# Performance work log

Measured on AMD Instinct MI355X. Metric: run time of the kernel, lower is better.

Reference implementation:

```python
import jax, jax.numpy as jnp
import numpy as np

ROPE_THETA = 10000.0


def rope(t, rot_dim):
    """lucidrains-style rotary embedding: rotate first rot_dim features,
    interleaved (x0,x1) pairing; remaining features pass through.
    t: [B, S, D] with rot_dim <= D."""
    S = t.shape[-2]
    half = rot_dim // 2
    inv_freq = 1.0 / (ROPE_THETA ** (jnp.arange(0, rot_dim, 2, dtype=jnp.float32) / rot_dim))  # [half]
    freqs = jnp.arange(S, dtype=jnp.float32)[:, None] * inv_freq[None, :]  # [S, half]
    freqs = jnp.repeat(freqs, 2, axis=-1)  # [S, rot_dim]
    cos, sin = jnp.cos(freqs), jnp.sin(freqs)
    t_rot, t_pass = t[..., :rot_dim], t[..., rot_dim:]
    x = t_rot.reshape(*t_rot.shape[:-1], half, 2)
    rh = jnp.stack([-x[..., 1], x[..., 0]], axis=-1).reshape(t_rot.shape)  # rotate_half (interleaved)
    t_rot = t_rot * cos + rh * sin
    return jnp.concatenate([t_rot, t_pass], axis=-1)


def feature_map(x):
    # L2 normalize along the feature dim (Hydra-attention canonical choice)
    norm = jnp.sqrt(jnp.sum(x * x, axis=-1, keepdims=True))
    return x / jnp.maximum(norm, 1e-12)


def setup_inputs() -> dict:
    key = jax.random.key(0)
    kx, kwi, kwo = jax.random.split(key, 3)
    B, S, D = 8, 4096, 2048
    scale = 0.02  # keep activations numerically tame
    return {
        "X": jax.random.normal(kx, (B, S, D), dtype=jnp.float32),
        "W_in": jax.random.normal(kwi, (3 * D, D), dtype=jnp.float32) * scale,
        "b_in": jnp.zeros((3 * D,), dtype=jnp.float32),
        "W_out": jax.random.normal(kwo, (D, D), dtype=jnp.float32) * scale,
        "b_out": jnp.zeros((D,), dtype=jnp.float32),
    }


def reference(X, W_in, b_in, W_out, b_out):
    D = X.shape[-1]
    QKV = jnp.einsum("bsd,ed->bse", X, W_in) + b_in  # [B, S, 3D]
    Q, K, V = jnp.split(QKV, 3, axis=-1)
    rot_dim = D // 2  # RotaryEmbedding(feature_dim // 2)
    Q = rope(Q, rot_dim)
    K = rope(K, rot_dim)
    A = jnp.sum(feature_map(K) * V, axis=-2)  # [B, D] global sum over sequence
    Y = A[:, None, :] * Q  # [B, S, D]
    Y = jnp.einsum("bsd,ed->bse", Y, W_out) + b_out
    return Y + X
```

## Files before the change

kernel.cpp:

```cpp
#include <hip/hip_runtime.h>

#define N_TOK   32768L
#define DMODEL  2048L
#define E1      6144L
#define ROT     1024
#define SMASK   4095

typedef __attribute__((ext_vector_type(8))) _Float16 half8;
typedef __attribute__((ext_vector_type(4))) _Float16 half4;
typedef __attribute__((ext_vector_type(4))) float    floatx4;
typedef __attribute__((ext_vector_type(4))) float    float4v;

__device__ inline void gld16(const void* g, void* l) {
  __builtin_amdgcn_global_load_lds(
      (const __attribute__((address_space(1))) unsigned int*)g,
      (__attribute__((address_space(3))) unsigned int*)l,
      16, 0, 0);
}

__global__ __launch_bounds__(256) void k_f2h(const float* __restrict__ in,
                                             _Float16* __restrict__ out,
                                             long nElem) {
  long i = ((long)blockIdx.x * 256 + threadIdx.x) * 4;
  if (i + 3 < nElem) {
    float4v v = *(const float4v*)(in + i);
    half4 o;
    o[0] = (_Float16)v[0]; o[1] = (_Float16)v[1];
    o[2] = (_Float16)v[2]; o[3] = (_Float16)v[3];
    *(half4*)(out + i) = o;
  }
}

__global__ __launch_bounds__(256) void k_zero(float* __restrict__ p, int n) {
  int i = blockIdx.x * 256 + threadIdx.x;
  if (i < n) p[i] = 0.f;
}

__global__ __launch_bounds__(256) void k_tab(float2* __restrict__ tab) {
  int i = blockIdx.x * 256 + threadIdx.x;
  int s = i >> 9, j = i & 511;
  float invf = (float)pow(10000.0, -(double)j / 512.0);
  float ang  = (float)s * invf;
  double sd, cd; sincos((double)ang, &sd, &cd);
  float2 o; o.x = (float)cd; o.y = (float)sd;
  tab[i] = o;
}


#define MM(qm, qn) do { \
  _Pragma("unroll") for (int m4 = 0; m4 < 4; m4++) \
  _Pragma("unroll") for (int n2 = 0; n2 < 2; n2++) { \
    acc[(qm)*4+m4][(qn)*2+n2] = __builtin_amdgcn_mfma_f32_16x16x32_f16( \
        af[m4][0], bf[n2][0], acc[(qm)*4+m4][(qn)*2+n2], 0, 0, 0); \
    acc[(qm)*4+m4][(qn)*2+n2] = __builtin_amdgcn_mfma_f32_16x16x32_f16( \
        af[m4][1], bf[n2][1], acc[(qm)*4+m4][(qn)*2+n2], 0, 0, 0); \
  } } while (0)

#define LD_A(buf, qm) do { \
  const _Float16* pA_ = &As[(buf)*16384 + (qm)*8192 + baseA]; \
  _Pragma("unroll") for (int m4 = 0; m4 < 4; m4++) { \
    af[m4][0] = *(const half8*)(pA_ + m4*1024 + okA0); \
    af[m4][1] = *(const half8*)(pA_ + m4*1024 + okA1); \
  } } while (0)

#define LD_B(buf, qn) do { \
  const _Float16* pB_ = &Bs[(buf)*16384 + (qn)*8192 + baseB]; \
  _Pragma("unroll") for (int n2 = 0; n2 < 2; n2++) { \
    bf[n2][0] = *(const half8*)(pB_ + n2*1024 + okB0); \
    bf[n2][1] = *(const half8*)(pB_ + n2*1024 + okB1); \
  } } while (0)

#define STG_A(buf, h, kt) do { \
  const _Float16* gA_ = gA + (long)(h)*128*LDA + (long)(kt)*64; \
  gld16(gA_,          dA + (buf)*16384 + (h)*8192); \
  gld16(gA_ + 8*LDA,  dA + (buf)*16384 + (h)*8192 + 512); \
  } while (0)

#define STG_B(buf, h, kt) do { \
  const _Float16* gB_ = gB + (long)(h)*128*2048 + (long)(kt)*64; \
  gld16(gB_,          dB + (buf)*16384 + (h)*8192); \
  gld16(gB_ + 8*2048, dB + (buf)*16384 + (h)*8192 + 512); \
  } while (0)

#define VM4  asm volatile("s_waitcnt vmcnt(4)" ::: "memory")
#define VM0  asm volatile("s_waitcnt vmcnt(0)" ::: "memory")
#define NOP_ ((void)0)

#define PHASE(LDRD, STG, MMA_, WV) do { \
  LDRD; STG; \
  asm volatile("" ::: "memory"); \
  __builtin_amdgcn_s_barrier(); \
  asm volatile("s_waitcnt lgkmcnt(0)" ::: "memory"); \
  __builtin_amdgcn_sched_barrier(0); \
  __builtin_amdgcn_s_setprio(1); \
  MMA_; \
  __builtin_amdgcn_s_setprio(0); \
  WV; \
  asm volatile("" ::: "memory"); \
  __builtin_amdgcn_s_barrier(); \
  asm volatile("" ::: "memory"); \
  } while (0)

template <int EB, long LDA, long LDC, bool FP32OUT>
__global__ __launch_bounds__(512, 2) void k_gemm256(
    const _Float16* __restrict__ Ag, const _Float16* __restrict__ Bg,
    const float* __restrict__ bias, const float* __restrict__ Xres,
    void* __restrict__ Cout) {
  __shared__ _Float16 As[32768];
  __shared__ _Float16 Bs[32768];

  const int t    = threadIdx.x;
  const int w    = t >> 6;
  const int l    = t & 63;
  const int quad = l >> 4;
  const int ln   = l & 15;
  const int wr   = w >> 2;
  const int wc   = w & 3;

  const int nwg = 128 * EB;
  const int bid = ((int)blockIdx.x & 7) * (nwg >> 3) + ((int)blockIdx.x >> 3);
  const int eb  = bid % EB;
  const int mb  = bid / EB;
  const long mRow0 = (long)mb * 256;
  const long eCol0 = (long)eb * 256;

  const int stR = (w << 4) + (l >> 3);
  const int stC = ((l & 7) ^ (l >> 3)) << 3;
  const _Float16* gA = Ag + (mRow0 + stR) * LDA  + stC;
  const _Float16* gB = Bg + (eCol0 + stR) * 2048 + stC;
  _Float16* dA = &As[(w * 128 + l) * 8];
  _Float16* dB = &Bs[(w * 128 + l) * 8];

  const int rA = (wr << 6) + ln;
  const int rB = (wc << 5) + ln;
  const int baseA = rA * 64;
  const int baseB = rB * 64;
  const int okA0 = ((quad    ) ^ (rA & 7)) << 3;
  const int okA1 = ((quad ^ 4) ^ (rA & 7)) << 3;
  const int okB0 = ((quad    ) ^ (rB & 7)) << 3;
  const int okB1 = ((quad ^ 4) ^ (rB & 7)) << 3;

  floatx4 acc[8][4];
#pragma unroll
  for (int i = 0; i < 8; i++)
#pragma unroll
    for (int j = 0; j < 4; j++) acc[i][j] = (floatx4){0.f, 0.f, 0.f, 0.f};
  half8 af[4][2], bf[2][2];

  STG_A(0, 0, 0); STG_B(0, 0, 0); STG_A(0, 1, 0); STG_B(0, 1, 0);
  STG_B(1, 0, 1); STG_A(1, 1, 1);
  VM4;
  asm volatile("" ::: "memory");
  __builtin_amdgcn_s_barrier();
  asm volatile("" ::: "memory");

#pragma unroll 1
  for (int it = 0; it < 15; ++it) {
    const int T = it * 2;
    PHASE({ LD_A(0,0); LD_B(0,0); }, STG_A(1,0,T+1), MM(0,0), NOP_);
    PHASE(LD_A(0,1),                 STG_B(1,1,T+1), MM(1,0), NOP_);
    PHASE(LD_B(0,1),                 STG_A(0,1,T+2), MM(1,1), NOP_);
    PHASE(LD_A(0,0),                 STG_B(0,0,T+2), MM(0,1), VM4);
    PHASE({ LD_A(1,0); LD_B(1,0); }, STG_A(0,0,T+2), MM(0,0), NOP_);
    PHASE(LD_A(1,1),                 STG_B(0,1,T+2), MM(1,0), NOP_);
    PHASE(LD_B(1,1),                 STG_B(1,0,T+3), MM(1,1), NOP_);
    PHASE(LD_A(1,0),                 STG_A(1,1,T+3), MM(0,1), VM4);
  }
  PHASE({ LD_A(0,0); LD_B(0,0); }, STG_A(1,0,31), MM(0,0), NOP_);
  PHASE(LD_A(0,1),                 STG_B(1,1,31), MM(1,0), NOP_);
  PHASE(LD_B(0,1),                 NOP_,          MM(1,1), NOP_);
  PHASE(LD_A(0,0),                 NOP_,          MM(0,1), VM0);
  PHASE({ LD_A(1,0); LD_B(1,0); }, NOP_,          MM(0,0), NOP_);
  PHASE(LD_A(1,1),                 NOP_,          MM(1,0), NOP_);
  PHASE(LD_B(1,1),                 NOP_,          MM(1,1), NOP_);
  PHASE(LD_A(1,0),                 NOP_,          MM(0,1), NOP_);

#pragma unroll
  for (int nt = 0; nt < 4; nt++) {
    const long e = eCol0 + ((nt >> 1) * 128 + (wc << 5) + ((nt & 1) << 4) + ln);
    const float bi = bias[e];
#pragma unroll
    for (int mt = 0; mt < 8; mt++) {
      const long m0 = mRow0 +
          ((mt >> 2) * 128 + (wr << 6) + ((mt & 3) << 4) + (quad << 2));
#pragma unroll
      for (int r = 0; r < 4; r++) {
        const long m = m0 + r;
        if constexpr (FP32OUT) {
          ((float*)Cout)[m * LDC + e] = acc[mt][nt][r] + bi + Xres[m * LDC + e];
        } else {
          ((_Float16*)Cout)[m * LDC + e] = (_Float16)(acc[mt][nt][r] + bi);
        }
      }
    }
  }
}

__global__ __launch_bounds__(256) void k_reduce_a(
    const _Float16* __restrict__ QKV, const float2* __restrict__ tab,
    float* __restrict__ A) {
  const int t  = threadIdx.x;
  const int w  = t >> 6;
  const int l  = t & 63;
  const int wg = blockIdx.x * 4 + w;
  const long row0 = (long)wg * 16;
  const int b  = (int)(row0 >> 12);
  const int d0 = l * 32;

  float acc[32];
  for (int j = 0; j < 32; j++) acc[j] = 0.f;

  for (int i = 0; i < 16; i++) {
    const long n = row0 + i;
    const int  s = (int)(n & SMASK);
    const _Float16* Kr = QKV + n * E1 + DMODEL     + d0;
    const _Float16* Vr = QKV + n * E1 + 2 * DMODEL + d0;
    float kx[32];
    for (int c = 0; c < 4; c++) {
      half8 h = *(const half8*)(Kr + c * 8);
      for (int j = 0; j < 8; j++) kx[c * 8 + j] = (float)h[j];
    }
    if (d0 < ROT) {
      const float2* trow = tab + ((long)s << 9) + (d0 >> 1);
      for (int p = 0; p < 16; p++) {
        float2 cs2 = trow[p];
        float x0 = kx[2 * p], x1 = kx[2 * p + 1];
        kx[2 * p]     = x0 * cs2.x - x1 * cs2.y;
        kx[2 * p + 1] = x1 * cs2.x + x0 * cs2.y;
      }
    }
    float ss = 0.f;
    for (int j = 0; j < 32; j++) ss += kx[j] * kx[j];
    for (int off = 32; off; off >>= 1) ss += __shfl_xor(ss, off);
    const float sc = 1.0f / fmaxf(sqrtf(ss), 1e-12f);
    for (int c = 0; c < 4; c++) {
      half8 h = *(const half8*)(Vr + c * 8);
      for (int j = 0; j < 8; j++)
        acc[c * 8 + j] += kx[c * 8 + j] * sc * (float)h[j];
    }
  }
  float* Ap = A + (long)b * DMODEL + d0;
  for (int j = 0; j < 32; j++) atomicAdd(&Ap[j], acc[j]);
}

__global__ __launch_bounds__(256) void k_make_y1(
    _Float16* __restrict__ QKV, const float2* __restrict__ tab,
    const float* __restrict__ A) {
  const long idx = (long)blockIdx.x * 256 + threadIdx.x;
  const long n   = idx >> 8;
  const int  c   = (int)(idx & 255);
  const int  d   = c * 8;
  const int  b   = (int)(n >> 12);
  const int  s   = (int)(n & SMASK);
  _Float16* Qp = QKV + n * E1 + d;
  half8 h = *(half8*)Qp;
  float x[8];
  for (int j = 0; j < 8; j++) x[j] = (float)h[j];
  if (d < ROT) {
    const float2* trow = tab + ((long)s << 9) + (d >> 1);
    for (int p = 0; p < 4; p++) {
      float2 cs2 = trow[p];
      float x0 = x[2 * p], x1 = x[2 * p + 1];
      x[2 * p]     = x0 * cs2.x - x1 * cs2.y;
      x[2 * p + 1] = x1 * cs2.x + x0 * cs2.y;
    }
  }
  const float* Ap = A + (long)b * DMODEL + d;
  for (int j = 0; j < 8; j++) x[j] *= Ap[j];
  half8 o;
  for (int j = 0; j < 8; j++) o[j] = (_Float16)x[j];
  *(half8*)Qp = o;
}

extern "C" void kernel_launch(void* const* d_in, const int* in_sizes, int n_in,
                              void* d_out, int out_size, void* d_ws, size_t ws_size,
                              hipStream_t stream) {
  const float* X     = (const float*)d_in[0];
  const float* W_in  = (const float*)d_in[1];
  const float* b_in  = (const float*)d_in[2];
  const float* W_out = (const float*)d_in[3];
  const float* b_out = (const float*)d_in[4];
  float* Out = (float*)d_out;

  char* ws = (char*)d_ws;
  _Float16* Xh  = (_Float16*)(ws);
  _Float16* W1h = (_Float16*)(ws + 134217728L);
  _Float16* W2h = (_Float16*)(ws + 159383552L);
  _Float16* QKV = (_Float16*)(ws + 167772160L);
  float*    A   = (float*)  (ws + 570425344L);
  float2*   TAB = (float2*)(ws);

  k_f2h<<<65536, 256, 0, stream>>>(X,     Xh,  N_TOK * DMODEL);
  k_f2h<<<12288, 256, 0, stream>>>(W_in,  W1h, E1 * DMODEL);
  k_f2h<<< 4096, 256, 0, stream>>>(W_out, W2h, DMODEL * DMODEL);
  k_zero<<<64, 256, 0, stream>>>(A, 8 * (int)DMODEL);

  k_gemm256<24, 2048L, 6144L, false><<<3072, 512, 0, stream>>>(
      Xh, W1h, b_in, nullptr, QKV);
  k_tab<<<8192, 256, 0, stream>>>(TAB);
  k_reduce_a<<<512, 256, 0, stream>>>(QKV, TAB, A);
  k_make_y1<<<32768, 256, 0, stream>>>(QKV, TAB, A);
  k_gemm256<8, 6144L, 2048L, true><<<1024, 512, 0, stream>>>(
      QKV, W2h, b_out, X, Out);
}
```

Baseline: 2.005 ms.

## Reorder GEMM phase schedule to deepen global prefetch and traverse sub-tiles in snake order

Reworks the 8-phase software pipeline of the 256x256 fp16 GEMM. Global-to-LDS staging now runs one more load ahead, with the wait relaxed from vmcnt(4) to vmcnt(6), and the prologue issues an extra stage. The MFMA sub-tile order changes to a serpentine (0,0)->(0,1)->(1,1)->(1,0) so consecutive phases reuse a fragment and only reload A or B. An lgkmcnt(8) hint is added on the first phase of each half. The goal is to hide more memory latency and cut LDS fragment reloads. The risk is a race if the reordered stage and buffer targets overwrite data that is still being read.

Result: faster. 1.935 ms (-3.5%).

```diff
diff --git a/kernel.cpp b/kernel.cpp
--- a/kernel.cpp
+++ b/kernel.cpp
@@ -82,12 +82,13 @@
   gld16(gB_ + 8*2048, dB + (buf)*16384 + (h)*8192 + 512); \
   } while (0)
 
-#define VM4  asm volatile("s_waitcnt vmcnt(4)" ::: "memory")
+#define VM6  asm volatile("s_waitcnt vmcnt(6)" ::: "memory")
 #define VM0  asm volatile("s_waitcnt vmcnt(0)" ::: "memory")
+#define LG8  asm volatile("s_waitcnt lgkmcnt(8)" ::: "memory")
 #define NOP_ ((void)0)
 
-#define PHASE(LDRD, STG, MMA_, WV) do { \
-  LDRD; STG; \
+#define PHASE(LDRD, STG, HINT, MMA_, WV) do { \
+  LDRD; STG; HINT; \
   asm volatile("" ::: "memory"); \
   __builtin_amdgcn_s_barrier(); \
   asm volatile("s_waitcnt lgkmcnt(0)" ::: "memory"); \
@@ -147,9 +148,9 @@
     for (int j = 0; j < 4; j++) acc[i][j] = (floatx4){0.f, 0.f, 0.f, 0.f};
   half8 af[4][2], bf[2][2];
 
-  STG_A(0, 0, 0); STG_B(0, 0, 0); STG_A(0, 1, 0); STG_B(0, 1, 0);
-  STG_B(1, 0, 1); STG_A(1, 1, 1);
-  VM4;
+  STG_A(0, 0, 0); STG_B(0, 0, 0); STG_B(0, 1, 0); STG_A(0, 1, 0);
+  STG_A(1, 0, 1); STG_B(1, 1, 1); STG_A(1, 1, 1);
+  VM6;
   asm volatile("" ::: "memory");
   __builtin_amdgcn_s_barrier();
   asm volatile("" ::: "memory");
@@ -157,23 +158,23 @@
 #pragma unroll 1
   for (int it = 0; it < 15; ++it) {
     const int T = it * 2;
-    PHASE({ LD_A(0,0); LD_B(0,0); }, STG_A(1,0,T+1), MM(0,0), NOP_);
-    PHASE(LD_A(0,1),                 STG_B(1,1,T+1), MM(1,0), NOP_);
-    PHASE(LD_B(0,1),                 STG_A(0,1,T+2), MM(1,1), NOP_);
-    PHASE(LD_A(0,0),                 STG_B(0,0,T+2), MM(0,1), VM4);
-    PHASE({ LD_A(1,0); LD_B(1,0); }, STG_A(0,0,T+2), MM(0,0), NOP_);
-    PHASE(LD_A(1,1),                 STG_B(0,1,T+2), MM(1,0), NOP_);
-    PHASE(LD_B(1,1),                 STG_B(1,0,T+3), MM(1,1), NOP_);
-    PHASE(LD_A(1,0),                 STG_A(1,1,T+3), MM(0,1), VM4);
-  }
-  PHASE({ LD_A(0,0); LD_B(0,0); }, STG_A(1,0,31), MM(0,0), NOP_);
-  PHASE(LD_A(0,1),                 STG_B(1,1,31), MM(1,0), NOP_);
-  PHASE(LD_B(0,1),                 NOP_,          MM(1,1), NOP_);
-  PHASE(LD_A(0,0),                 NOP_,          MM(0,1), VM0);
-  PHASE({ LD_A(1,0); LD_B(1,0); }, NOP_,          MM(0,0), NOP_);
-  PHASE(LD_A(1,1),                 NOP_,          MM(1,0), NOP_);
-  PHASE(LD_B(1,1),                 NOP_,          MM(1,1), NOP_);
-  PHASE(LD_A(1,0),                 NOP_,          MM(0,1), NOP_);
+    PHASE({ LD_A(0,0); LD_B(0,0); }, STG_B(1,0,T+1), LG8,  MM(0,0), NOP_);
+    PHASE(LD_B(0,1),                 STG_A(0,0,T+2), NOP_, MM(0,1), NOP_);
+    PHASE(LD_A(0,1),                 STG_B(0,1,T+2), NOP_, MM(1,1), NOP_);
+    PHASE(LD_B(0,0),                 STG_A(0,1,T+2), NOP_, MM(1,0), VM6);
+    PHASE({ LD_A(1,0); LD_B(1,0); }, STG_B(0,0,T+2), LG8,  MM(0,0), NOP_);
+    PHASE(LD_B(1,1),                 STG_A(1,0,T+3), NOP_, MM(0,1), NOP_);
+    PHASE(LD_A(1,1),                 STG_B(1,1,T+3), NOP_, MM(1,1), NOP_);
+    PHASE(LD_B(1,0),                 STG_A(1,1,T+3), NOP_, MM(1,0), VM6);
+  }
+  PHASE({ LD_A(0,0); LD_B(0,0); }, STG_B(1,0,31), LG8,  MM(0,0), NOP_);
+  PHASE(LD_B(0,1),                 NOP_,          NOP_, MM(0,1), NOP_);
+  PHASE(LD_A(0,1),                 NOP_,          NOP_, MM(1,1), NOP_);
+  PHASE(LD_B(0,0),                 NOP_,          NOP_, MM(1,0), VM0);
+  PHASE({ LD_A(1,0); LD_B(1,0); }, NOP_,          LG8,  MM(0,0), NOP_);
+  PHASE(LD_B(1,1),                 NOP_,          NOP_, MM(0,1), NOP_);
+  PHASE(LD_A(1,1),                 NOP_,          NOP_, MM(1,1), NOP_);
+  PHASE(LD_B(1,0),                 NOP_,          NOP_, MM(1,0), NOP_);
 
 #pragma unroll
   for (int nt = 0; nt < 4; nt++) {
```
